# Kernel optimization log

Hardware: AMD Instinct MI355X
Metric: run time of the kernel (lower is better)

The kernel has to match this reference:

```python
import jax, jax.numpy as jnp
import numpy as np
from functools import partial

B, S, A = 128, 256, 8
V, E, H, C, HOPS = 50000, 300, 300, 3, 3

def _lstm_dir(x, lens, Wih, Whh, bih, bhh):
    # x: [B,S,E]; masked (packed-style) LSTM: padded steps don't update state, output 0
    b, s, _ = x.shape
    h_dim = Whh.shape[1]
    xg = jnp.einsum('bse,ge->bsg', x, Wih) + bih  # [B,S,4H]
    mask = (jnp.arange(s)[None, :] < lens[:, None])  # [B,S]

    def step(carry, inp):
        h, c = carry
        xg_t, m = inp  # [B,4H], [B]
        g = xg_t + h @ Whh.T + bhh
        i, f, gg, o = jnp.split(g, 4, axis=-1)
        i = jax.nn.sigmoid(i); f = jax.nn.sigmoid(f)
        gg = jnp.tanh(gg); o = jax.nn.sigmoid(o)
        c_new = f * c + i * gg
        h_new = o * jnp.tanh(c_new)
        m2 = m[:, None]
        h2 = jnp.where(m2, h_new, h)
        c2 = jnp.where(m2, c_new, c)
        out = jnp.where(m2, h_new, 0.0)
        return (h2, c2), out

    z = jnp.zeros((b, h_dim), x.dtype)
    _, outs = jax.lax.scan(step, (z, z), (xg.transpose(1, 0, 2), mask.T))
    return outs.transpose(1, 0, 2)

def _bilstm(x, lens, Wih_f, Whh_f, bih_f, bhh_f, Wih_b, Whh_b, bih_b, bhh_b):
    out_f = _lstm_dir(x, lens, Wih_f, Whh_f, bih_f, bhh_f)
    s = x.shape[1]
    t = jnp.arange(s)[None, :]
    # reverse each sequence within its own valid length
    idx = jnp.where(t < lens[:, None], lens[:, None] - 1 - t, t)  # [B,S]
    x_rev = jnp.take_along_axis(x, idx[:, :, None], axis=1)
    out_b_rev = _lstm_dir(x_rev, lens, Wih_b, Whh_b, bih_b, bhh_b)
    out_b = jnp.take_along_axis(out_b_rev, idx[:, :, None], axis=1)
    return jnp.concatenate([out_f, out_b], axis=-1)  # [B,S,2H]

def _locationed_memory(memory, mem_len, left_len, asp_len):
    b, s, _ = memory.shape
    pos = jnp.arange(s, dtype=memory.dtype)[None, :]  # [1,S]
    ml = mem_len[:, None].astype(memory.dtype)
    ll = left_len[:, None].astype(memory.dtype)
    al = asp_len[:, None].astype(memory.dtype)
    in_left = pos < ll
    in_right = (pos >= ll + al) & (pos < ml)
    w = jnp.where(in_left, 1.0 - (ll - pos) / ml,
        jnp.where(in_right, 1.0 - (pos - ll - al + 1.0) / ml, 1.0))
    u = jnp.where(in_left, pos - ll,
        jnp.where(in_right, pos - ll - al + 1.0, 0.0))
    v = memory * w[:, :, None]
    return jnp.concatenate([v, u[:, :, None]], axis=2)  # [B,S,2H+1]

def _gru_cell(x, h, Wih, Whh, bih, bhh):
    gi = x @ Wih.T + bih
    gh = h @ Whh.T + bhh
    i_r, i_z, i_n = jnp.split(gi, 3, axis=-1)
    h_r, h_z, h_n = jnp.split(gh, 3, axis=-1)
    r = jax.nn.sigmoid(i_r + h_r)
    z = jax.nn.sigmoid(i_z + h_z)
    n = jnp.tanh(i_n + r * h_n)
    return (1.0 - z) * n + z * h

def setup_inputs() -> dict:
    key = jax.random.key(0)
    ks = jax.random.split(key, 24)
    mem_len = jax.random.randint(ks[0], (B,), S // 2, S + 1)
    asp_len = jax.random.randint(ks[1], (B,), 1, A + 1)
    max_left = mem_len - asp_len
    left_len = jax.random.randint(ks[2], (B,), 0, 10**6) % (max_left + 1)

    def make_ids(k, n, lens):
        tok = jax.random.randint(k, (B, n), 1, V)
        return jnp.where(jnp.arange(n)[None, :] < lens[:, None], tok, 0)

    text = make_ids(ks[3], S, mem_len)
    aspect = make_ids(ks[4], A, asp_len)
    left_context = make_ids(ks[5], S, left_len)

    def nrm(k, shape, scale=0.05):
        return jax.random.normal(k, shape, jnp.float32) * scale

    params = dict(
        embedding=nrm(ks[6], (V, E), 0.1),
        Wih_f=nrm(ks[7], (4 * H, E)), Whh_f=nrm(ks[8], (4 * H, H)),
        bih_f=nrm(ks[9], (4 * H,)), bhh_f=nrm(ks[10], (4 * H,)),
        Wih_b=nrm(ks[11], (4 * H, E)), Whh_b=nrm(ks[12], (4 * H, H)),
        bih_b=nrm(ks[13], (4 * H,)), bhh_b=nrm(ks[14], (4 * H,)),
        att_W=nrm(ks[15], (1, 2 * H + 1 + 2 * E)), att_b=nrm(ks[16], (1,)),
        gru_Wih=nrm(ks[17], (3 * E, 2 * H + 1)), gru_Whh=nrm(ks[18], (3 * E, E)),
        gru_bih=nrm(ks[19], (3 * E,)), gru_bhh=nrm(ks[20], (3 * E,)),
        dense_W=nrm(ks[21], (C, E)), dense_b=nrm(ks[22], (C,)),
    )
    return dict(text=text, aspect=aspect, left_context=left_context, **params)

def reference(text, aspect, left_context, embedding,
              Wih_f, Whh_f, bih_f, bhh_f, Wih_b, Whh_b, bih_b, bhh_b,
              att_W, att_b, gru_Wih, gru_Whh, gru_bih, gru_bhh,
              dense_W, dense_b):
    left_len = jnp.sum(left_context != 0, axis=-1)
    mem_len = jnp.sum(text != 0, axis=-1)
    asp_len = jnp.sum(aspect != 0, axis=-1)

    memory = embedding[text]  # [B,S,E]
    memory = _bilstm(memory, mem_len, Wih_f, Whh_f, bih_f, bhh_f,
                     Wih_b, Whh_b, bih_b, bhh_b)  # [B,S,2H]
    memory = _locationed_memory(memory, mem_len, left_len, asp_len)  # [B,S,2H+1]

    asp_emb = jnp.sum(embedding[aspect], axis=1) / asp_len[:, None].astype(jnp.float32)  # [B,E]

    et = jnp.zeros_like(asp_emb)
    b, s, _ = memory.shape
    for _ in range(HOPS):
        a = jnp.concatenate([
            memory,
            jnp.broadcast_to(et[:, None, :], (b, s, et.shape[-1])),
            jnp.broadcast_to(asp_emb[:, None, :], (b, s, asp_emb.shape[-1])),
        ], axis=-1)  # [B,S,2H+1+2E]
        g = jnp.einsum('bsd,od->bso', a, att_W) + att_b  # [B,S,1]
        alpha = jax.nn.softmax(g, axis=1)
        i = jnp.einsum('bso,bsd->bd', alpha, memory)  # [B,2H+1]
        et = _gru_cell(i, et, gru_Wih, gru_Whh, gru_bih, gru_bhh)
    return et @ dense_W.T + dense_b  # [B,C]
```

## Files before the change

### kernel.cpp

```cpp
#include <hip/hip_runtime.h>
#include <hip/hip_bf16.h>
#include <math.h>

#define B_ 128
#define S_ 256
#define A_ 8
#define E_ 300
#define H_ 300
#define KPAD 320
#define NGU 16
#define NCOL 80
#define HROW 328
#define NBLK 128
#define GST 82

typedef unsigned short u16;
typedef unsigned int u32;
typedef unsigned long long u64;
typedef __attribute__((ext_vector_type(8))) short short8;
typedef __attribute__((ext_vector_type(4))) float floatx4;
typedef __attribute__((ext_vector_type(4))) unsigned int u32x4;

#define MFMA16(a, b, c) __builtin_amdgcn_mfma_f32_16x16x32_bf16((a), (b), (c), 0, 0, 0)
#define LD4_SC0(d, a) asm volatile("global_load_dwordx4 %0, %1, off sc0" : "=v"(d) : "v"(a) : "memory")
#define LD2_SC0(d, a) asm volatile("global_load_dwordx2 %0, %1, off sc0" : "=v"(d) : "v"(a) : "memory")

__device__ __host__ __forceinline__ int gu_cnt(int g) { return g < 6 ? 20 : 18; }
__device__ __host__ __forceinline__ int gu_u0(int g) { return g < 6 ? 20 * g : 120 + 18 * (g - 6); }

static constexpr size_t oLens = 0;
static constexpr size_t oMemX = 331776;
static constexpr size_t oWp   = 42274816;
static constexpr size_t oBp   = 45551616;
static constexpr size_t oMemV = 45561856;
static constexpr size_t oIT   = 124205056;
static constexpr size_t oGi   = 124512768;
static constexpr size_t oGh   = 124973568;
static constexpr size_t oEt   = 125434368;
static constexpr size_t oSc   = 125587968;
static constexpr size_t oHTP  = 125719040;
static constexpr size_t oHTS  = 126374400;
static constexpr size_t WS_NEED = 127029760;

__device__ __forceinline__ u16 f2bf(float f) {
  union { float f; unsigned u; } v; v.f = f;
  unsigned r = (v.u + 0x7FFFu + ((v.u >> 16) & 1u)) >> 16;
  return (u16)r;
}
__device__ __forceinline__ float sigm(float x) { return 1.f / (1.f + __expf(-x)); }
__device__ __forceinline__ float tanh_f(float x) {
  x = fminf(15.f, fmaxf(-15.f, x));
  float e = __expf(2.f * x);
  return (e - 1.f) / (e + 1.f);
}

__device__ __forceinline__ bool tags_ok(const u32x4 (&q)[10], u32 tgv, int scol0) {
  bool ok = true;
  #pragma unroll
  for (int i = 0; i < 10; ++i) {
    ok = ok && ((q[i][1] == tgv) || (scol0 + 2 * i >= 150));
    ok = ok && ((q[i][3] == tgv) || (scol0 + 2 * i + 1 >= 150));
  }
  return ok;
}
__device__ __forceinline__ void load_plain(u32x4 (&q)[10], const u64* sp) {
  #pragma unroll
  for (int i = 0; i < 10; ++i) LD4_SC0(q[i], sp + 2 * i);
}
__device__ __forceinline__ void load_mirror(u32x4 (&q)[10], const u64* sp) {
  #pragma unroll
  for (int i = 0; i < 10; ++i) {
    u64 lo = __hip_atomic_load(sp + 2 * i, __ATOMIC_RELAXED, __HIP_MEMORY_SCOPE_AGENT);
    u64 hi = __hip_atomic_load(sp + 2 * i + 1, __ATOMIC_RELAXED, __HIP_MEMORY_SCOPE_AGENT);
    q[i] = (u32x4){(u32)lo, (u32)(lo >> 32), (u32)hi, (u32)(hi >> 32)};
  }
}

__global__ __launch_bounds__(256) void init_kernel(const int* __restrict__ text,
                                                   const int* __restrict__ aspect,
                                                   const int* __restrict__ leftc,
                                                   char* __restrict__ ws) {
  const int bid = blockIdx.x, tid = threadIdx.x;
  if (bid == 0) {
    if (tid < B_) {
      int c = 0; const int* p = text + tid * S_;
      for (int s = 0; s < S_; ++s) c += (p[s] != 0);
      ((int*)(ws + oLens))[tid] = c;
    }
  } else if (bid == 1) {
    if (tid < B_) {
      int c = 0; const int* p = leftc + tid * S_;
      for (int s = 0; s < S_; ++s) c += (p[s] != 0);
      ((int*)(ws + oLens + 512))[tid] = c;
    }
  } else if (bid == 2) {
    if (tid < B_) {
      int c = 0; const int* p = aspect + tid * A_;
      for (int s = 0; s < A_; ++s) c += (p[s] != 0);
      ((int*)(ws + oLens + 1024))[tid] = c;
    }
  } else {
    const int T1 = 163840, T2 = 163840, EW = 38400;
    const int total = T1 + T2 + EW;
    for (int i = (bid - 3) * 256 + tid; i < total; i += 64 * 256) {
      int j = i;
      if (j < T1) { ((u32*)(ws + oHTP))[j] = 0u; continue; }  j -= T1;
      if (j < T2) { ((u32*)(ws + oHTS))[j] = 0u; continue; }  j -= T2;
      ((u32*)(ws + oEt))[j] = 0u;
    }
  }
}

__global__ __launch_bounds__(256) void pack_kernel(
    const float* __restrict__ WihF, const float* __restrict__ WhhF,
    const float* __restrict__ bihF, const float* __restrict__ bhhF,
    const float* __restrict__ WihB, const float* __restrict__ WhhB,
    const float* __restrict__ bihB, const float* __restrict__ bhhB,
    char* __restrict__ ws) {
  const int WTOT = 2 * NGU * NCOL * 640;
  int idx = blockIdx.x * 256 + threadIdx.x;
  if (idx < WTOT) {
    int k = idx % 640;
    int n = (idx / 640) % NCOL;
    int g = (idx / (640 * NCOL)) % NGU;
    int dir = idx / (640 * NCOL * NGU);
    float v = 0.f;
    const int cnt = gu_cnt(g), u0 = gu_u0(g);
    if (n < cnt * 4) {
      int col = (n & 3) * 300 + u0 + (n >> 2);
      const float* Wih = dir ? WihB : WihF;
      const float* Whh = dir ? WhhB : WhhF;
      if (k < 300)                  v = Wih[(size_t)col * 300 + k];
      else if (k >= 320 && k < 620) v = Whh[(size_t)col * 300 + (k - 320)];
    }
    ((u16*)(ws + oWp))[idx] = f2bf(v);
  } else {
    int j = idx - WTOT;
    if (j < 2 * NGU * NCOL) {
      int n = j % NCOL; int g = (j / NCOL) % NGU; int dir = j / (NCOL * NGU);
      float v = 0.f;
      const int cnt = gu_cnt(g), u0 = gu_u0(g);
      if (n < cnt * 4) {
        int col = (n & 3) * 300 + u0 + (n >> 2);
        v = (dir ? bihB : bihF)[col] + (dir ? bhhB : bhhF)[col];
      }
      ((float*)(ws + oBp))[j] = v;
    }
  }
}

__global__ __launch_bounds__(KPAD) void gather_kernel(const int* __restrict__ text,
                                                      const float* __restrict__ emb,
                                                      char* __restrict__ ws) {
  const int bid = blockIdx.x;
  const int t = bid & 255;
  const int b = (bid >> 8) & 127;
  const int dir = bid >> 15;
  const int len = ((const int*)(ws + oLens))[b];
  const int tp = (dir == 0) ? t : ((t < len) ? (len - 1 - t) : t);
  const int tok = text[b * S_ + tp];
  u16* dst = (u16*)(ws + oMemX) + ((size_t)((dir * B_ + b) * S_ + t)) * KPAD;
  const float* src = emb + (size_t)tok * E_;
  const int k = threadIdx.x;
  float v = (k < E_) ? src[k] : 0.f;
  dst[k] = f2bf(v);
}

__global__ __launch_bounds__(256, 1) void lstm_kernel(char* __restrict__ ws) {
  const int bid = (int)blockIdx.x;
  const int pod = bid & 7;
  const int dir = pod >> 2;
  const int gb  = pod & 3;
  const int g   = bid >> 3;
  const int cnt = gu_cnt(g), u0 = gu_u0(g);
  const int npair = cnt >> 1;
  const int tid = threadIdx.x;
  const int wv = tid >> 6;
  const int lane = tid & 63;
  const int quad = lane >> 4;
  const int l16 = lane & 15;
  const int Mtile = wv >> 1;
  const int nt0 = (wv & 1) ? 3 : 0;
  const int ntc = (wv & 1) ? 2 : 3;

  const u16* __restrict__ Wg = (const u16*)(ws + oWp) + (size_t)(dir * NGU + g) * NCOL * 640;
  const float* __restrict__ Bpk = (const float*)(ws + oBp) + (dir * NGU + g) * NCOL;
  const u16* __restrict__ memx = (const u16*)(ws + oMemX) + (size_t)dir * B_ * S_ * KPAD;
  u64* __restrict__ hTP = (u64*)(ws + oHTP);
  u64* __restrict__ hTS = (u64*)(ws + oHTS);
  float* __restrict__ memv = (float*)(ws + oMemV);

  __shared__ __align__(16) u16 hLds[32 * HROW];
  __shared__ float gatesLds[32 * GST];
  __shared__ float cS[640];
  __shared__ float hS[640];
  __shared__ float biasS[NCOL];
  __shared__ int lenS[32], llS[32], alS[32];

  for (int i = tid; i < 640; i += 256) { cS[i] = 0.f; hS[i] = 0.f; }
  for (int i = tid; i < 32 * HROW / 2; i += 256) ((u32*)hLds)[i] = 0u;
  if (tid < NCOL) biasS[tid] = Bpk[tid];
  if (tid < 32) {
    lenS[tid] = ((const int*)(ws + oLens))[gb * 32 + tid];
    llS[tid]  = ((const int*)(ws + oLens + 512))[gb * 32 + tid];
    alS[tid]  = ((const int*)(ws + oLens + 1024))[gb * 32 + tid];
  }

  short8 wx[10][3], wh[10][3];
  #pragma unroll
  for (int kk = 0; kk < 10; ++kk) {
    #pragma unroll
    for (int j = 0; j < 3; ++j) {
      if (j < ntc) {
        const u16* base = Wg + (size_t)((nt0 + j) * 16 + l16) * 640 + quad * 8;
        wx[kk][j] = *(const short8*)(base + kk * 32);
        wh[kk][j] = *(const short8*)(base + 320 + kk * 32);
      }
    }
  }
  __syncthreads();

  const int row = gb * 32 + Mtile * 16 + l16;
  const u16* hA = hLds + (Mtile * 16 + l16) * HROW + quad * 8;

  const int srow = tid >> 3;
  const int scol0 = (tid & 7) * 20;
  u16* sdst = hLds + srow * HROW + scol0 * 2;
  const size_t sboff = (size_t)(gb * 32 + srow) * 160 + scol0;
  const size_t sentoff = (size_t)(gb * 32) * 160 + (lane < 6 ? 10 * lane : 60 + 9 * (lane - 6));

  short8 xv[10];
  {
    const u16* xr = memx + ((size_t)row * S_) * KPAD + quad * 8;
    #pragma unroll
    for (int kk = 0; kk < 10; ++kk) xv[kk] = *(const short8*)(xr + kk * 32);
  }

  for (int t = 0; t < S_; ++t) {
    const size_t parbase = ((size_t)(t & 1) * 2 + dir) * (B_ * 160);

    if (t > 0) {
      if (wv == 0) {
        const u64* saP = hTP + parbase + sentoff;
        const u64* saS = hTS + parbase + sentoff;
        const u32 tgv = (u32)t;
        while (true) {
          u64 svP = 0, svS = 0;
          if (lane < NGU) {
            LD2_SC0(svP, saP);
            svS = __hip_atomic_load(saS, __ATOMIC_RELAXED, __HIP_MEMORY_SCOPE_AGENT);
          }
          asm volatile("s_waitcnt vmcnt(0)" ::: "memory");
          __builtin_amdgcn_sched_barrier(0);
          bool ok = (lane >= NGU) || ((u32)(svP >> 32) == tgv) || ((u32)(svS >> 32) == tgv);
          if (__all((int)ok)) break;
        }
      }
      asm volatile("s_barrier" ::: "memory");
    }

    u32x4 q[10];
    if (t > 0) load_plain(q, hTP + parbase + sboff);

    floatx4 acc[3];
    acc[0] = (floatx4){0.f, 0.f, 0.f, 0.f}; acc[1] = acc[0]; acc[2] = acc[0];
    #pragma unroll
    for (int kk = 0; kk < 10; ++kk) {
      #pragma unroll
      for (int j = 0; j < 3; ++j) {
        if (j < ntc)
          acc[j] = MFMA16(xv[kk], wx[kk][j], acc[j]);
      }
    }

    if (t > 0) {
      const u32 tgv = (u32)t;
      int tries = 0;
      asm volatile("s_waitcnt vmcnt(0)" ::: "memory");
      __builtin_amdgcn_sched_barrier(0);
      while (!tags_ok(q, tgv, scol0)) {
        ++tries;
        if (tries <= 2) load_plain(q, hTP + parbase + sboff);
        else            load_mirror(q, hTS + parbase + sboff);
        asm volatile("s_waitcnt vmcnt(0)" ::: "memory");
        __builtin_amdgcn_sched_barrier(0);
      }
      #pragma unroll
      for (int i = 0; i < 10; i += 2) {
        u32x4 pk = (u32x4){q[i][0], q[i][2], q[i + 1][0], q[i + 1][2]};
        *(u32x4*)(sdst + 4 * i) = pk;
      }
    }

    asm volatile("s_waitcnt lgkmcnt(0)" ::: "memory");
    asm volatile("s_barrier" ::: "memory");

    #pragma unroll
    for (int kk = 0; kk < 10; ++kk) {
      const short8 av = *(const short8*)(hA + kk * 32);
      #pragma unroll
      for (int j = 0; j < 3; ++j) {
        if (j < ntc)
          acc[j] = MFMA16(av, wh[kk][j], acc[j]);
      }
    }

    #pragma unroll
    for (int j = 0; j < 3; ++j) {
      if (j < ntc) {
        const int colb = (nt0 + j) * 16 + l16;
        const int rb = Mtile * 16 + quad * 4;
        #pragma unroll
        for (int r = 0; r < 4; ++r)
          gatesLds[(rb + r) * GST + colb] = acc[j][r];
      }
    }
    asm volatile("s_waitcnt lgkmcnt(0)" ::: "memory");
    asm volatile("s_barrier" ::: "memory");

    #pragma unroll
    for (int z = 0; z < 2; ++z) {
      const int it = tid + z * 256;
      if (it < 32 * npair) {
        const int bl = it & 31;
        const int pl = it >> 5;
        const int ul0 = pl * 2;
        const int len = lenS[bl];
        const bool m = (t < len);
        const float* gp = gatesLds + bl * GST + ul0 * 4;
        const float* bp = biasS + ul0 * 4;
        float h0K, h1K, h0N, h1N;
        {
          float ig = sigm(gp[0] + bp[0]);
          float fg = sigm(gp[1] + bp[1]);
          float gt = tanh_f(gp[2] + bp[2]);
          float og = sigm(gp[3] + bp[3]);
          float cOld = cS[ul0 * 32 + bl], hOld = hS[ul0 * 32 + bl];
          float cNew = fg * cOld + ig * gt;
          float hNew = og * tanh_f(cNew);
          cS[ul0 * 32 + bl] = m ? cNew : cOld;
          h0K = m ? hNew : hOld;
          hS[ul0 * 32 + bl] = h0K;
          h0N = m ? hNew : 0.f;
        }
        {
          float ig = sigm(gp[4] + bp[4]);
          float fg = sigm(gp[5] + bp[5]);
          float gt = tanh_f(gp[6] + bp[6]);
          float og = sigm(gp[7] + bp[7]);
          float cOld = cS[(ul0 + 1) * 32 + bl], hOld = hS[(ul0 + 1) * 32 + bl];
          float cNew = fg * cOld + ig * gt;
          float hNew = og * tanh_f(cNew);
          cS[(ul0 + 1) * 32 + bl] = m ? cNew : cOld;
          h1K = m ? hNew : hOld;
          hS[(ul0 + 1) * 32 + bl] = h1K;
          h1N = m ? hNew : 0.f;
        }
        const int bglob = gb * 32 + bl;
        u32 packed = (u32)f2bf(h0K) | ((u32)f2bf(h1K) << 16);
        u64 tg64 = (u64)packed | ((u64)(u32)(t + 1) << 32);
        const size_t hx = ((size_t)((t + 1) & 1) * 2 + dir) * (B_ * 160)
                        + (size_t)bglob * 160 + ((u0 + ul0) >> 1);
        *(volatile u64*)(hTP + hx) = tg64;
        __hip_atomic_store(&hTS[hx], tg64,
                           __ATOMIC_RELAXED, __HIP_MEMORY_SCOPE_AGENT);
        int pos = (dir == 0) ? t : (m ? (len - 1 - t) : t);
        float ml = (float)len, ll = (float)llS[bl], al = (float)alS[bl];
        float p = (float)pos;
        float wl;
        if (p < ll) wl = 1.f - (ll - p) / ml;
        else if ((p >= ll + al) && (p < ml)) wl = 1.f - (p - ll - al + 1.f) / ml;
        else wl = 1.f;
        *(float2*)&memv[((size_t)bglob * S_ + pos) * 600 + dir * 300 + u0 + ul0] =
            make_float2(h0N * wl, h1N * wl);
      }
    }

    if (t + 1 < S_) {
      const u16* xr = memx + ((size_t)row * S_ + (t + 1)) * KPAD + quad * 8;
      #pragma unroll
      for (int kk = 0; kk < 10; ++kk) xv[kk] = *(const short8*)(xr + kk * 32);
    }
  }
}

__global__ __launch_bounds__(256) void score_kernel(const float* __restrict__ attW,
                                                    char* __restrict__ ws) {
  const int bid = blockIdx.x;
  const int b = bid >> 1, sh = bid & 1;
  const int tid = threadIdx.x, wv = tid >> 6, lane = tid & 63;
  __shared__ float aW[601];
  for (int i = tid; i < 601; i += 256) aW[i] = attW[i];
  const float* memv = (const float*)(ws + oMemV) + (size_t)b * S_ * 600;
  const float ml = (float)((const int*)(ws + oLens))[b];
  const float ll = (float)((const int*)(ws + oLens + 512))[b];
  const float al = (float)((const int*)(ws + oLens + 1024))[b];
  __syncthreads();
  float* scg = (float*)(ws + oSc) + b * S_;
  for (int s = sh * 128 + wv; s < sh * 128 + 128; s += 4) {
    const float* rowp = memv + (size_t)s * 600;
    float acc = 0.f;
    for (int d = lane; d < 600; d += 64) acc += rowp[d] * aW[d];
    for (int off = 32; off; off >>= 1) acc += __shfl_xor(acc, off);
    if (lane == 0) {
      float p = (float)s;
      bool inl = p < ll;
      bool inr = (p >= ll + al) && (p < ml);
      float u = inl ? (p - ll) : (inr ? (p - ll - al + 1.f) : 0.f);
      scg[s] = acc + u * aW[600];
    }
  }
}

__global__ __launch_bounds__(256) void attn_kernel(char* __restrict__ ws) {
  const int bid = blockIdx.x;
  const int b = bid >> 1, dh = bid & 1;
  const int tid = threadIdx.x, wv = tid >> 6, lane = tid & 63;
  __shared__ float alpha[256];
  __shared__ float red[8];
  const float* scg = (const float*)(ws + oSc) + b * S_;
  float v = scg[tid];
  float mx = v;
  for (int off = 32; off; off >>= 1) mx = fmaxf(mx, __shfl_xor(mx, off));
  if (lane == 0) red[wv] = mx;
  __syncthreads();
  mx = fmaxf(fmaxf(red[0], red[1]), fmaxf(red[2], red[3]));
  float e = __expf(v - mx);
  float sm = e;
  for (int off = 32; off; off >>= 1) sm += __shfl_xor(sm, off);
  if (lane == 0) red[4 + wv] = sm;
  __syncthreads();
  float tot = red[4] + red[5] + red[6] + red[7];
  alpha[tid] = e / tot;
  const float ml = (float)((const int*)(ws + oLens))[b];
  const float ll = (float)((const int*)(ws + oLens + 512))[b];
  const float al = (float)((const int*)(ws + oLens + 1024))[b];
  __syncthreads();
  const float* memv = (const float*)(ws + oMemV) + (size_t)b * S_ * 600;
  float* iT = (float*)(ws + oIT);
  const int d0 = dh * 301, d1 = dh ? 601 : 301;
  for (int d = d0 + tid; d < d1; d += 256) {
    float acc = 0.f;
    if (d < 600) {
      for (int s = 0; s < 256; ++s) acc += alpha[s] * memv[(size_t)s * 600 + d];
    } else {
      for (int s = 0; s < 256; ++s) {
        float p = (float)s;
        bool inl = p < ll;
        bool inr = (p >= ll + al) && (p < ml);
        float u = inl ? (p - ll) : (inr ? (p - ll - al + 1.f) : 0.f);
        acc += alpha[s] * u;
      }
    }
    iT[d * 128 + b] = acc;
  }
}

__global__ __launch_bounds__(256) void gi_kernel(const float* __restrict__ Wih,
                                                 const float* __restrict__ bih,
                                                 char* __restrict__ ws) {
  int idx = blockIdx.x * 256 + threadIdx.x;
  int r = idx >> 7, b = idx & 127;
  if (r >= 900) return;
  const float* iT = (const float*)(ws + oIT);
  const float* wr = Wih + (size_t)r * 601;
  float acc = bih[r];
  for (int d = 0; d < 601; ++d) acc += iT[d * 128 + b] * wr[d];
  ((float*)(ws + oGi))[r * 128 + b] = acc;
}

__global__ __launch_bounds__(256) void gh_kernel(const float* __restrict__ Whh,
                                                 const float* __restrict__ bhh,
                                                 char* __restrict__ ws) {
  int idx = blockIdx.x * 256 + threadIdx.x;
  int r = idx >> 7, b = idx & 127;
  if (r >= 900) return;
  const float* et = (const float*)(ws + oEt);
  const float* wr = Whh + (size_t)r * 300;
  float acc = bhh[r];
  for (int u = 0; u < 300; ++u) acc += et[u * 128 + b] * wr[u];
  ((float*)(ws + oGh))[r * 128 + b] = acc;
}

__global__ __launch_bounds__(256) void up_kernel(char* __restrict__ ws) {
  int idx = blockIdx.x * 256 + threadIdx.x;
  int u = idx >> 7, b = idx & 127;
  if (u >= 300) return;
  const float* gi = (const float*)(ws + oGi);
  const float* gh = (const float*)(ws + oGh);
  float* et = (float*)(ws + oEt);
  float rr = sigm(gi[u * 128 + b] + gh[u * 128 + b]);
  float zz = sigm(gi[(300 + u) * 128 + b] + gh[(300 + u) * 128 + b]);
  float nn = tanh_f(gi[(600 + u) * 128 + b] + rr * gh[(600 + u) * 128 + b]);
  float old = et[u * 128 + b];
  et[u * 128 + b] = (1.f - zz) * nn + zz * old;
}

__global__ __launch_bounds__(384) void dense_kernel(const float* __restrict__ dW,
                                                    const float* __restrict__ dB,
                                                    float* __restrict__ out,
                                                    const char* __restrict__ ws) {
  int tid = threadIdx.x;
  if (tid >= 384) return;
  int b = tid / 3, c = tid - 3 * (tid / 3);
  const float* et = (const float*)(ws + oEt);
  float acc = dB[c];
  const float* wr = dW + c * 300;
  for (int u = 0; u < 300; ++u) acc += et[u * 128 + b] * wr[u];
  out[b * 3 + c] = acc;
}

extern "C" void kernel_launch(void* const* d_in, const int* in_sizes, int n_in,
                              void* d_out, int out_size, void* d_ws, size_t ws_size,
                              hipStream_t stream) {
  const int* text = (const int*)d_in[0];
  const int* aspect = (const int*)d_in[1];
  const int* leftc = (const int*)d_in[2];
  const float* emb = (const float*)d_in[3];
  const float* WihF = (const float*)d_in[4];
  const float* WhhF = (const float*)d_in[5];
  const float* bihF = (const float*)d_in[6];
  const float* bhhF = (const float*)d_in[7];
  const float* WihB = (const float*)d_in[8];
  const float* WhhB = (const float*)d_in[9];
  const float* bihB = (const float*)d_in[10];
  const float* bhhB = (const float*)d_in[11];
  const float* attW = (const float*)d_in[12];
  const float* gruWih = (const float*)d_in[14];
  const float* gruWhh = (const float*)d_in[15];
  const float* gruBih = (const float*)d_in[16];
  const float* gruBhh = (const float*)d_in[17];
  const float* denseW = (const float*)d_in[18];
  const float* denseB = (const float*)d_in[19];
  float* out = (float*)d_out;
  char* ws = (char*)d_ws;
  if (ws_size < WS_NEED) return;

  init_kernel<<<67, 256, 0, stream>>>(text, aspect, leftc, ws);
  pack_kernel<<<6420, 256, 0, stream>>>(WihF, WhhF, bihF, bhhF, WihB, WhhB, bihB, bhhB, ws);
  gather_kernel<<<2 * B_ * S_, KPAD, 0, stream>>>(text, emb, ws);
  lstm_kernel<<<NBLK, 256, 0, stream>>>(ws);
  score_kernel<<<2 * B_, 256, 0, stream>>>(attW, ws);
  attn_kernel<<<2 * B_, 256, 0, stream>>>(ws);
  gi_kernel<<<450, 256, 0, stream>>>(gruWih, gruBih, ws);
  for (int h = 0; h < 3; ++h) {
    gh_kernel<<<450, 256, 0, stream>>>(gruWhh, gruBhh, ws);
    up_kernel<<<150, 256, 0, stream>>>(ws);
  }
  dense_kernel<<<1, 384, 0, stream>>>(denseW, denseB, out, ws);
}
```

Before: 2.107 ms.

## Load recurrent h operands directly from global into MFMA registers, skipping LDS staging

Each lane now fetches its own MFMA A-operand fragments of the tagged h exchange buffer straight from global memory and checks the tags per fragment. This removes the cooperative load, the LDS write, a block barrier and the LDS re-read on every timestep. The spin-wait polls only the primary buffer and checks the mirror every eighth iteration, which cuts atomic traffic. In exchange there are redundant global loads, because waves sharing an M tile read the same rows, and more VGPR pressure from the twenty uint4 registers per lane.

Result: slower. 2.815 ms (+33.6%).

```diff
diff --git a/kernel.cpp b/kernel.cpp
--- a/kernel.cpp
+++ b/kernel.cpp
@@ -10,7 +10,6 @@
 #define KPAD 320
 #define NGU 16
 #define NCOL 80
-#define HROW 328
 #define NBLK 128
 #define GST 82
 
@@ -52,28 +51,6 @@
   x = fminf(15.f, fmaxf(-15.f, x));
   float e = __expf(2.f * x);
   return (e - 1.f) / (e + 1.f);
-}
-
-__device__ __forceinline__ bool tags_ok(const u32x4 (&q)[10], u32 tgv, int scol0) {
-  bool ok = true;
-  #pragma unroll
-  for (int i = 0; i < 10; ++i) {
-    ok = ok && ((q[i][1] == tgv) || (scol0 + 2 * i >= 150));
-    ok = ok && ((q[i][3] == tgv) || (scol0 + 2 * i + 1 >= 150));
-  }
-  return ok;
-}
-__device__ __forceinline__ void load_plain(u32x4 (&q)[10], const u64* sp) {
-  #pragma unroll
-  for (int i = 0; i < 10; ++i) LD4_SC0(q[i], sp + 2 * i);
-}
-__device__ __forceinline__ void load_mirror(u32x4 (&q)[10], const u64* sp) {
-  #pragma unroll
-  for (int i = 0; i < 10; ++i) {
-    u64 lo = __hip_atomic_load(sp + 2 * i, __ATOMIC_RELAXED, __HIP_MEMORY_SCOPE_AGENT);
-    u64 hi = __hip_atomic_load(sp + 2 * i + 1, __ATOMIC_RELAXED, __HIP_MEMORY_SCOPE_AGENT);
-    q[i] = (u32x4){(u32)lo, (u32)(lo >> 32), (u32)hi, (u32)(hi >> 32)};
-  }
 }
 
 __global__ __launch_bounds__(256) void init_kernel(const int* __restrict__ text,
@@ -190,7 +167,6 @@
   u64* __restrict__ hTS = (u64*)(ws + oHTS);
   float* __restrict__ memv = (float*)(ws + oMemV);
 
-  __shared__ __align__(16) u16 hLds[32 * HROW];
   __shared__ float gatesLds[32 * GST];
   __shared__ float cS[640];
   __shared__ float hS[640];
@@ -198,7 +174,6 @@
   __shared__ int lenS[32], llS[32], alS[32];
 
   for (int i = tid; i < 640; i += 256) { cS[i] = 0.f; hS[i] = 0.f; }
-  for (int i = tid; i < 32 * HROW / 2; i += 256) ((u32*)hLds)[i] = 0u;
   if (tid < NCOL) biasS[tid] = Bpk[tid];
   if (tid < 32) {
     lenS[tid] = ((const int*)(ws + oLens))[gb * 32 + tid];
@@ -220,18 +195,12 @@
   }
   __syncthreads();
 
-  const int row = gb * 32 + Mtile * 16 + l16;
-  const u16* hA = hLds + (Mtile * 16 + l16) * HROW + quad * 8;
-
-  const int srow = tid >> 3;
-  const int scol0 = (tid & 7) * 20;
-  u16* sdst = hLds + srow * HROW + scol0 * 2;
-  const size_t sboff = (size_t)(gb * 32 + srow) * 160 + scol0;
+  const int arow = gb * 32 + Mtile * 16 + l16;
   const size_t sentoff = (size_t)(gb * 32) * 160 + (lane < 6 ? 10 * lane : 60 + 9 * (lane - 6));
 
   short8 xv[10];
   {
-    const u16* xr = memx + ((size_t)row * S_) * KPAD + quad * 8;
+    const u16* xr = memx + ((size_t)arow * S_) * KPAD + quad * 8;
     #pragma unroll
     for (int kk = 0; kk < 10; ++kk) xv[kk] = *(const short8*)(xr + kk * 32);
   }
@@ -244,23 +213,36 @@
         const u64* saP = hTP + parbase + sentoff;
         const u64* saS = hTS + parbase + sentoff;
         const u32 tgv = (u32)t;
+        int itc = 0;
         while (true) {
-          u64 svP = 0, svS = 0;
-          if (lane < NGU) {
-            LD2_SC0(svP, saP);
-            svS = __hip_atomic_load(saS, __ATOMIC_RELAXED, __HIP_MEMORY_SCOPE_AGENT);
-          }
+          u64 svP = 0;
+          if (lane < NGU) LD2_SC0(svP, saP);
           asm volatile("s_waitcnt vmcnt(0)" ::: "memory");
           __builtin_amdgcn_sched_barrier(0);
-          bool ok = (lane >= NGU) || ((u32)(svP >> 32) == tgv) || ((u32)(svS >> 32) == tgv);
+          bool ok = (lane >= NGU) || ((u32)(svP >> 32) == tgv);
           if (__all((int)ok)) break;
+          if ((++itc & 7) == 0) {
+            u64 svS = 0;
+            if (lane < NGU)
+              svS = __hip_atomic_load(saS, __ATOMIC_RELAXED, __HIP_MEMORY_SCOPE_AGENT);
+            bool ok2 = (lane >= NGU) || ((u32)(svP >> 32) == tgv) || ((u32)(svS >> 32) == tgv);
+            if (__all((int)ok2)) break;
+          }
         }
       }
       asm volatile("s_barrier" ::: "memory");
     }
 
-    u32x4 q[10];
-    if (t > 0) load_plain(q, hTP + parbase + sboff);
+    u32x4 qa[10], qb[10];
+    if (t > 0) {
+      const u64* hrow = hTP + parbase + (size_t)arow * 160;
+      #pragma unroll
+      for (int kk = 0; kk < 10; ++kk) {
+        const int wb = quad * 4 + kk * 16;
+        LD4_SC0(qa[kk], hrow + wb);
+        LD4_SC0(qb[kk], hrow + wb + 2);
+      }
+    }
 
     floatx4 acc[3];
     acc[0] = (floatx4){0.f, 0.f, 0.f, 0.f}; acc[1] = acc[0]; acc[2] = acc[0];
@@ -275,33 +257,55 @@
 
     if (t > 0) {
       const u32 tgv = (u32)t;
-      int tries = 0;
       asm volatile("s_waitcnt vmcnt(0)" ::: "memory");
       __builtin_amdgcn_sched_barrier(0);
-      while (!tags_ok(q, tgv, scol0)) {
+      int tries = 0;
+      while (true) {
+        bool ok = true;
+        #pragma unroll
+        for (int kk = 0; kk < 10; ++kk) {
+          const int wb = quad * 4 + kk * 16;
+          ok = ok && ((qa[kk][1] == tgv) || (wb + 0 >= 150));
+          ok = ok && ((qa[kk][3] == tgv) || (wb + 1 >= 150));
+          ok = ok && ((qb[kk][1] == tgv) || (wb + 2 >= 150));
+          ok = ok && ((qb[kk][3] == tgv) || (wb + 3 >= 150));
+        }
+        if (ok) break;
         ++tries;
-        if (tries <= 2) load_plain(q, hTP + parbase + sboff);
-        else            load_mirror(q, hTS + parbase + sboff);
+        if (tries <= 2) {
+          const u64* hrow = hTP + parbase + (size_t)arow * 160;
+          #pragma unroll
+          for (int kk = 0; kk < 10; ++kk) {
+            const int wb = quad * 4 + kk * 16;
+            LD4_SC0(qa[kk], hrow + wb);
+            LD4_SC0(qb[kk], hrow + wb + 2);
+          }
+        } else {
+          const u64* hrow = hTS + parbase + (size_t)arow * 160;
+          #pragma unroll
+          for (int kk = 0; kk < 10; ++kk) {
+            const int wb = quad * 4 + kk * 16;
+            u64 a0 = __hip_atomic_load(hrow + wb + 0, __ATOMIC_RELAXED, __HIP_MEMORY_SCOPE_AGENT);
+            u64 a1 = __hip_atomic_load(hrow + wb + 1, __ATOMIC_RELAXED, __HIP_MEMORY_SCOPE_AGENT);
+            u64 a2 = __hip_atomic_load(hrow + wb + 2, __ATOMIC_RELAXED, __HIP_MEMORY_SCOPE_AGENT);
+            u64 a3 = __hip_atomic_load(hrow + wb + 3, __ATOMIC_RELAXED, __HIP_MEMORY_SCOPE_AGENT);
+            qa[kk] = (u32x4){(u32)a0, (u32)(a0 >> 32), (u32)a1, (u32)(a1 >> 32)};
+            qb[kk] = (u32x4){(u32)a2, (u32)(a2 >> 32), (u32)a3, (u32)(a3 >> 32)};
+          }
+        }
         asm volatile("s_waitcnt vmcnt(0)" ::: "memory");
         __builtin_amdgcn_sched_barrier(0);
       }
+
       #pragma unroll
-      for (int i = 0; i < 10; i += 2) {
-        u32x4 pk = (u32x4){q[i][0], q[i][2], q[i + 1][0], q[i + 1][2]};
-        *(u32x4*)(sdst + 4 * i) = pk;
-      }
-    }
-
-    asm volatile("s_waitcnt lgkmcnt(0)" ::: "memory");
-    asm volatile("s_barrier" ::: "memory");
-
-    #pragma unroll
-    for (int kk = 0; kk < 10; ++kk) {
-      const short8 av = *(const short8*)(hA + kk * 32);
-      #pragma unroll
-      for (int j = 0; j < 3; ++j) {
-        if (j < ntc)
-          acc[j] = MFMA16(av, wh[kk][j], acc[j]);
+      for (int kk = 0; kk < 10; ++kk) {
+        u32x4 pk = (u32x4){qa[kk][0], qa[kk][2], qb[kk][0], qb[kk][2]};
+        const short8 av = *(const short8*)&pk;
+        #pragma unroll
+        for (int j = 0; j < 3; ++j) {
+          if (j < ntc)
+            acc[j] = MFMA16(av, wh[kk][j], acc[j]);
+        }
       }
     }
 
@@ -377,7 +381,7 @@
     }
 
     if (t + 1 < S_) {
-      const u16* xr = memx + ((size_t)row * S_ + (t + 1)) * KPAD + quad * 8;
+      const u16* xr = memx + ((size_t)arow * S_ + (t + 1)) * KPAD + quad * 8;
       #pragma unroll
       for (int kk = 0; kk < 10; ++kk) xv[kk] = *(const short8*)(xr + kk * 32);
     }
```
